# Kernel optimization log

Hardware: AMD Instinct MI355X
Metric: run time of the kernel (lower is better)

## Reference

```python
import jax, jax.numpy as jnp
import numpy as np

B, N, IN_DIM, OUT_DIM, H = 8, 1024, 256, 256, 4
HD = OUT_DIM // H  # head_dim = 64
NEG = -1e9
EPS = 1e-5


def setup_inputs() -> dict:
    key = jax.random.key(0)
    ks = jax.random.split(key, 9)
    h = jax.random.normal(ks[0], (B, N, IN_DIM), dtype=jnp.float32)
    adj = jax.random.randint(ks[1], (N, N), 0, 2, dtype=jnp.int32)
    adj = adj.at[jnp.arange(N), jnp.arange(N)].set(1)  # self loops so no empty rows
    s = 1.0 / np.sqrt(IN_DIM)
    W = jax.random.uniform(ks[2], (H, IN_DIM, HD), jnp.float32, -s, s)
    sa = 1.0 / np.sqrt(2 * HD)
    a1 = jax.random.uniform(ks[3], (H, HD), jnp.float32, -sa, sa)
    a2 = jax.random.uniform(ks[4], (H, HD), jnp.float32, -sa, sa)
    sp = 1.0 / np.sqrt(OUT_DIM)
    proj_w = jax.random.uniform(ks[5], (OUT_DIM, OUT_DIM), jnp.float32, -sp, sp)
    proj_b = jax.random.uniform(ks[6], (OUT_DIM,), jnp.float32, -sp, sp)
    gamma = jnp.ones((OUT_DIM,), jnp.float32)
    beta = jnp.zeros((OUT_DIM,), jnp.float32)
    return {"h": h, "adj": adj, "W": W, "a1": a1, "a2": a2,
            "proj_w": proj_w, "proj_b": proj_b, "gamma": gamma, "beta": beta}


def reference(h, adj, W, a1, a2, proj_w, proj_b, gamma, beta):
    # Wh: [B,H,N,HD]
    Wh = jnp.einsum('bni,hid->bhnd', h, W)
    # Decompose a([Wh_i || Wh_j]) = a1.Wh_i + a2.Wh_j (same math as concat+linear)
    si = jnp.einsum('bhnd,hd->bhn', Wh, a1)  # [B,H,N]
    sj = jnp.einsum('bhnd,hd->bhn', Wh, a2)
    e = jax.nn.leaky_relu(si[:, :, :, None] + sj[:, :, None, :], 0.2)  # [B,H,N,N]
    mask = (adj == 0)  # [N,N]
    e = jnp.where(mask[None, None], NEG, e)
    alpha = jax.nn.softmax(e, axis=-1)
    out = jnp.einsum('bhnm,bhmd->bhnd', alpha, Wh)  # [B,H,N,HD]
    h_multi = out.transpose(0, 2, 1, 3).reshape(B, N, OUT_DIM)  # concat heads
    h_out = jnp.einsum('bnd,od->bno', h_multi, proj_w) + proj_b
    h_out = h_out + h  # residual (in_dim == out_dim)
    mu = jnp.mean(h_out, axis=-1, keepdims=True)
    var = jnp.mean(jnp.square(h_out - mu), axis=-1, keepdims=True)
    return (h_out - mu) * jax.lax.rsqrt(var + EPS) * gamma + beta
```

## Files before the change

kernel.cpp:

```cpp
#include <hip/hip_runtime.h>
#include <hip/hip_bf16.h>

#define NN 1024
#define LOG2E 1.44269504088896f

typedef __attribute__((ext_vector_type(8))) short short8;
typedef __attribute__((ext_vector_type(4))) float floatx4;
typedef __attribute__((ext_vector_type(4))) int intx4;
typedef __attribute__((ext_vector_type(2))) int intx2;

#define WAIT_VM0()   asm volatile("s_waitcnt vmcnt(0)" ::: "memory")
#define WAIT_VM4()   asm volatile("s_waitcnt vmcnt(4)" ::: "memory")
#define WAIT_LGKM0() asm volatile("s_waitcnt lgkmcnt(0)" ::: "memory")
#define SCHED_FENCE() asm volatile("" ::: "memory")

static __device__ __forceinline__ unsigned pk2(float f0, float f1) {
    unsigned u0 = __float_as_uint(f0) + 0x8000u;
    unsigned u1 = __float_as_uint(f1) + 0x8000u;
    return __builtin_amdgcn_perm(u1, u0, 0x07060302u);
}
static __device__ __forceinline__ short8 pk8(floatx4 v0, floatx4 v1) {
    union { intx4 i; short8 s; } u;
    u.i[0] = (int)pk2(v0[0], v0[1]); u.i[1] = (int)pk2(v0[2], v0[3]);
    u.i[2] = (int)pk2(v1[0], v1[1]); u.i[3] = (int)pk2(v1[2], v1[3]);
    return u.s;
}
static __device__ __forceinline__ void load_lds16(const void* gsrc, void* lds) {
    __builtin_amdgcn_global_load_lds(
        (const __attribute__((address_space(1))) void*)gsrc,
        (__attribute__((address_space(3))) void*)lds, 16, 0, 0);
}

__global__ __launch_bounds__(256) void prep_kernel(
    const float* __restrict__ W, const float* __restrict__ proj_w,
    const int* __restrict__ adj,
    __hip_bfloat16* __restrict__ WTb,
    __hip_bfloat16* __restrict__ pwb,
    unsigned* __restrict__ adjm)
{
    int blk = blockIdx.x, t = threadIdx.x;
    if (blk < 16) {
        int o = blk * 16 + (t >> 4);
        int hh = o >> 6, d = o & 63;
        #pragma unroll
        for (int kk = 0; kk < 16; ++kk) {
            int k = (t & 15) + 16 * kk;
            WTb[(size_t)o * 256 + k] = __float2bfloat16(W[((size_t)hh * 256 + k) * 64 + d]);
        }
    } else if (blk < 32) {
        size_t base = (size_t)(blk - 16) * 4096 + (size_t)t * 16;
        #pragma unroll
        for (int k = 0; k < 16; k += 8) {
            floatx4 v0 = *(const floatx4*)(proj_w + base + k);
            floatx4 v1 = *(const floatx4*)(proj_w + base + k + 4);
            *(short8*)(pwb + base + k) = pk8(v0, v1);
        }
    } else {
        int n = (blk - 32) * 8 + (t >> 5);
        int wd = t & 31;
        const int* arow = adj + (size_t)n * NN + wd * 32;
        unsigned bits = 0;
        #pragma unroll
        for (int j4 = 0; j4 < 8; ++j4) {
            intx4 v = *(const intx4*)(arow + j4 * 4);
            #pragma unroll
            for (int j = 0; j < 4; ++j) if (v[j] != 0) bits |= (1u << (j4 * 4 + j));
        }
        adjm[(size_t)n * 32 + wd] = bits;
    }
}

__global__ __launch_bounds__(512) void wh_kernel(
    const float* __restrict__ h,
    const __hip_bfloat16* __restrict__ WTb,
    const float* __restrict__ a1, const float* __restrict__ a2,
    __hip_bfloat16* __restrict__ WhTt,
    float* __restrict__ si, float* __restrict__ sj)
{
    __shared__ __align__(16) __hip_bfloat16 WTbs[8][4096];
    __shared__ float redsi[2][4][4][16];
    __shared__ float redsj[2][4][4][16];

    int t = threadIdx.x;
    int w = t >> 6, l = t & 63;
    int rt = w >> 2, ds = w & 3;
    int rl = l & 15, q = l >> 4;
    int bx = blockIdx.x;
    int bb = bx >> 5, tb = bx & 31;

    short8 af[8];
    const float* Arow = h + ((size_t)bb * 1024 + tb * 32 + rt * 16 + rl) * 256 + q * 8;
    #pragma unroll
    for (int k0 = 0; k0 < 8; ++k0) {
        floatx4 v0 = *(const floatx4*)(Arow + k0 * 32);
        floatx4 v1 = *(const floatx4*)(Arow + k0 * 32 + 4);
        af[k0] = pk8(v0, v1);
    }

    int d = ds * 16 + rl;
    int s = rt * 16 + q * 4;
    size_t toff = (size_t)d * 32 + (((s >> 3) ^ (d & 3)) * 8) + (s & 7);
    int srow_ = l >> 5;

    #pragma unroll
    for (int ph = 0; ph < 2; ++ph) {
        if (ph) __syncthreads();
        #pragma unroll
        for (int k = 0; k < 8; ++k) {
            int row = k * 2 + srow_;
            int g = (l & 31) ^ (row & 7);
            load_lds16(WTb + (size_t)(ph * 128 + w * 16 + row) * 256 + g * 8, &WTbs[w][k * 512]);
        }
        __syncthreads();

        #pragma unroll
        for (int jj = 0; jj < 2; ++jj) {
            int head = ph * 2 + jj;
            int lt = ds + 4 * jj;
            floatx4 acc = {0.f, 0.f, 0.f, 0.f};
            #pragma unroll
            for (int k0 = 0; k0 < 8; ++k0) {
                int p = ((k0 << 2) + q) ^ (rl & 7);
                short8 bf = *(const short8*)(&WTbs[lt][rl * 256 + p * 8]);
                acc = __builtin_amdgcn_mfma_f32_16x16x32_bf16(af[k0], bf, acc, 0, 0, 0);
            }

            intx2 pr;
            pr[0] = (int)pk2(acc[0], acc[1]);
            pr[1] = (int)pk2(acc[2], acc[3]);
            *(intx2*)(WhTt + ((size_t)(bb * 4 + head) * 32 + tb) * 2048 + toff) = pr;

            float av1 = a1[head * 64 + d] * LOG2E;
            float av2 = a2[head * 64 + d] * LOG2E;
            #pragma unroll
            for (int i = 0; i < 4; ++i) {
                float p1 = acc[i] * av1, p2 = acc[i] * av2;
                #pragma unroll
                for (int off = 1; off < 16; off <<= 1) {
                    p1 += __shfl_xor(p1, off, 64);
                    p2 += __shfl_xor(p2, off, 64);
                }
                if (rl == 0) { redsi[rt][ds][head][q * 4 + i] = p1; redsj[rt][ds][head][q * 4 + i] = p2; }
            }
        }
    }
    __syncthreads();

    if (t < 128) {
        int head = t >> 5, u = t & 31, rt2 = u >> 4, row = u & 15;
        si[(size_t)(bb * 4 + head) * NN + tb * 32 + rt2 * 16 + row] =
            redsi[rt2][0][head][row] + redsi[rt2][1][head][row] +
            redsi[rt2][2][head][row] + redsi[rt2][3][head][row];
    } else if (t < 256) {
        int u2 = t - 128;
        int head = u2 >> 5, u = u2 & 31, rt2 = u >> 4, row = u & 15;
        sj[(size_t)(bb * 4 + head) * NN + tb * 32 + rt2 * 16 + row] =
            redsj[rt2][0][head][row] + redsj[rt2][1][head][row] +
            redsj[rt2][2][head][row] + redsj[rt2][3][head][row];
    }
}

__global__ __launch_bounds__(512, 4) void attn_proj_kernel(
    const unsigned* __restrict__ adjm,
    const __hip_bfloat16* __restrict__ WhTt,
    const float* __restrict__ si, const float* __restrict__ sj,
    const __hip_bfloat16* __restrict__ pwb,
    const float* __restrict__ h,
    const float* __restrict__ proj_b, const float* __restrict__ gamma,
    const float* __restrict__ beta,
    float* __restrict__ out)
{
    __shared__ __align__(16) char smem[76288];
    auto bst   = reinterpret_cast<__hip_bfloat16 (*)[2][2048]>(smem);
    auto pl    = reinterpret_cast<__hip_bfloat16 (*)[16][40]>(smem + 65536);
    auto hm    = reinterpret_cast<__hip_bfloat16 (*)[264]>(smem + 65536);
    auto red   = reinterpret_cast<float (*)[8][16]>(smem + 65536 + 8448);
    auto lsums = reinterpret_cast<float (*)[4][16]>(smem + 75776);
    float (*accx)[64][20] = reinterpret_cast<float (*)[64][20]>(smem);

    int bx = blockIdx.x, t = threadIdx.x;
    int w = t >> 6, l = t & 63;
    int hh = w & 3, e = w >> 2;
    int rl = l & 15, q = l >> 4;
    int b = bx >> 6, n0 = (bx & 63) * 16;
    int bh = b * 4 + hh;
    int r0 = bx * 16;

    int r = l >> 2, cg = l & 3;
    float sii = si[(size_t)bh * NN + n0 + r];
    const float* sjr = sj + (size_t)bh * NN;
    const unsigned* amrow = adjm + (size_t)(n0 + r) * 32;

    float lsum = 0.f;
    floatx4 acc[4] = { {0,0,0,0}, {0,0,0,0}, {0,0,0,0}, {0,0,0,0} };

    const __hip_bfloat16* Tbase = WhTt + ((size_t)bh * 32 + e) * 2048 + l * 8;

    #pragma unroll
    for (int k = 0; k < 4; ++k)
        load_lds16(Tbase + k * 512, &bst[w][0][k * 512]);

    #pragma unroll 2
    for (int it = 0; it < 16; ++it) {
        int buf = it & 1;
        int mw = it * 64 + e * 32;
        {
            unsigned bits = amrow[it * 2 + e] >> (cg * 8);
            int mb = mw + cg * 8;
            #pragma unroll
            for (int c4 = 0; c4 < 2; ++c4) {
                floatx4 s4 = *(const floatx4*)(sjr + mb + c4 * 4);
                float pv[4];
                #pragma unroll
                for (int k = 0; k < 4; ++k) {
                    float x = sii + s4[k];
                    x = fmaxf(x, 0.2f * x);
                    x = ((bits >> (c4 * 4 + k)) & 1u) ? x : -1e9f;
                    pv[k] = exp2f(x);
                    lsum += pv[k];
                }
                intx2 two;
                two[0] = (int)pk2(pv[0], pv[1]);
                two[1] = (int)pk2(pv[2], pv[3]);
                *(intx2*)(&pl[w][r][cg * 8 + c4 * 4]) = two;
            }
        }
        SCHED_FENCE();
        if (it < 15) {
            const __hip_bfloat16* Tn = Tbase + (size_t)(it + 1) * 2 * 2048;
            #pragma unroll
            for (int k = 0; k < 4; ++k)
                load_lds16(Tn + k * 512, &bst[w][buf ^ 1][k * 512]);
            WAIT_VM4();
        } else {
            WAIT_VM0();
        }
        short8 afr = *(const short8*)(&pl[w][rl][q * 8]);
        #pragma unroll
        for (int dt = 0; dt < 4; ++dt) {
            short8 bfr = *(const short8*)(&bst[w][buf][(dt * 16 + rl) * 32 + (q ^ (rl & 3)) * 8]);
            acc[dt] = __builtin_amdgcn_mfma_f32_16x16x32_bf16(afr, bfr, acc[dt], 0, 0, 0);
        }
    }

    lsum += __shfl_xor(lsum, 1, 64);
    lsum += __shfl_xor(lsum, 2, 64);
    if (cg == 0) lsums[e][hh][r] = lsum;

    __syncthreads();

    if (e == 1) {
        #pragma unroll
        for (int dt = 0; dt < 4; ++dt) {
            #pragma unroll
            for (int i = 0; i < 4; ++i)
                accx[hh][l][dt * 4 + i] = acc[dt][i];
        }
    }
    __syncthreads();

    if (e == 0) {
        float riv[4];
        #pragma unroll
        for (int i = 0; i < 4; ++i)
            riv[i] = 1.f / (lsums[0][hh][q * 4 + i] + lsums[1][hh][q * 4 + i]);
        #pragma unroll
        for (int dt = 0; dt < 4; ++dt) {
            #pragma unroll
            for (int i = 0; i < 4; ++i) {
                float v = acc[dt][i] + accx[hh][l][dt * 4 + i];
                unsigned uv = (__float_as_uint(v * riv[i]) + 0x8000u) >> 16;
                hm[q * 4 + i][hh * 64 + dt * 16 + rl] = __ushort_as_bfloat16((unsigned short)uv);
            }
        }
    }
    __syncthreads();

    short8 paf[8];
    #pragma unroll
    for (int k0 = 0; k0 < 8; ++k0) paf[k0] = *(const short8*)(&hm[rl][q * 8 + k0 * 32]);

    floatx4 pacc[2];
    #pragma unroll
    for (int j = 0; j < 2; ++j) {
        int ct = w + 8 * j;
        const __hip_bfloat16* Bp = pwb + (size_t)(ct * 16 + rl) * 256 + q * 8;
        floatx4 a = {0.f, 0.f, 0.f, 0.f};
        #pragma unroll
        for (int k0 = 0; k0 < 8; ++k0) {
            short8 bfp = *(const short8*)(Bp + k0 * 32);
            a = __builtin_amdgcn_mfma_f32_16x16x32_bf16(paf[k0], bfp, a, 0, 0, 0);
        }
        pacc[j] = a;
    }

    float ps[4] = {0.f, 0.f, 0.f, 0.f};
    #pragma unroll
    for (int j = 0; j < 2; ++j) {
        int col = (w + 8 * j) * 16 + rl;
        float pb = proj_b[col];
        #pragma unroll
        for (int i = 0; i < 4; ++i) {
            float v = pacc[j][i] + pb + h[(size_t)(r0 + q * 4 + i) * 256 + col];
            pacc[j][i] = v;
            ps[i] += v;
        }
    }
    #pragma unroll
    for (int i = 0; i < 4; ++i) {
        float s = ps[i];
        #pragma unroll
        for (int off = 1; off < 16; off <<= 1) s += __shfl_xor(s, off, 64);
        ps[i] = s;
    }
    if (rl == 0) {
        for (int i = 0; i < 4; ++i) red[0][w][q * 4 + i] = ps[i];
    }
    __syncthreads();
    float mu[4];
    #pragma unroll
    for (int i = 0; i < 4; ++i) {
        int row = q * 4 + i;
        float s = 0.f;
        #pragma unroll
        for (int ww = 0; ww < 8; ++ww) s += red[0][ww][row];
        mu[i] = s * (1.f / 256.f);
    }
    float vs[4] = {0.f, 0.f, 0.f, 0.f};
    #pragma unroll
    for (int j = 0; j < 2; ++j) {
        #pragma unroll
        for (int i = 0; i < 4; ++i) { float cv = pacc[j][i] - mu[i]; vs[i] += cv * cv; }
    }
    #pragma unroll
    for (int i = 0; i < 4; ++i) {
        float s = vs[i];
        #pragma unroll
        for (int off = 1; off < 16; off <<= 1) s += __shfl_xor(s, off, 64);
        vs[i] = s;
    }
    if (rl == 0) {
        for (int i = 0; i < 4; ++i) red[1][w][q * 4 + i] = vs[i];
    }
    __syncthreads();
    float rs[4];
    #pragma unroll
    for (int i = 0; i < 4; ++i) {
        int row = q * 4 + i;
        float s = 0.f;
        #pragma unroll
        for (int ww = 0; ww < 8; ++ww) s += red[1][ww][row];
        rs[i] = rsqrtf(s * (1.f / 256.f) + 1e-5f);
    }
    #pragma unroll
    for (int j = 0; j < 2; ++j) {
        int col = (w + 8 * j) * 16 + rl;
        float g = gamma[col], be = beta[col];
        #pragma unroll
        for (int i = 0; i < 4; ++i)
            out[(size_t)(r0 + q * 4 + i) * 256 + col] = (pacc[j][i] - mu[i]) * rs[i] * g + be;
    }
}

extern "C" void kernel_launch(void* const* d_in, const int* in_sizes, int n_in,
                              void* d_out, int out_size, void* d_ws, size_t ws_size,
                              hipStream_t stream) {
    const float* h      = (const float*)d_in[0];
    const int*   adj    = (const int*)d_in[1];
    const float* W      = (const float*)d_in[2];
    const float* a1     = (const float*)d_in[3];
    const float* a2     = (const float*)d_in[4];
    const float* proj_w = (const float*)d_in[5];
    const float* proj_b = (const float*)d_in[6];
    const float* gamma  = (const float*)d_in[7];
    const float* beta   = (const float*)d_in[8];
    float* out = (float*)d_out;

    char* ws = (char*)d_ws;
    __hip_bfloat16* WhTt = (__hip_bfloat16*)ws;  ws += (size_t)32 * 32 * 2048 * 2;
    __hip_bfloat16* WTb = (__hip_bfloat16*)ws;   ws += 256 * 256 * 2;
    __hip_bfloat16* pwb = (__hip_bfloat16*)ws;   ws += 256 * 256 * 2;
    float* si = (float*)ws;                      ws += (size_t)32 * NN * 4;
    float* sj = (float*)ws;                      ws += (size_t)32 * NN * 4;
    unsigned* adjm = (unsigned*)ws;              ws += (size_t)NN * 32 * 4;

    prep_kernel<<<160, 256, 0, stream>>>(W, proj_w, adj, WTb, pwb, adjm);
    wh_kernel<<<256, 512, 0, stream>>>(h, WTb, a1, a2, WhTt, si, sj);
    attn_proj_kernel<<<512, 512, 0, stream>>>(adjm, WhTt, si, sj, pwb, h, proj_b, gamma, beta, out);
}
```

Before: 120.5 us.

## Split fused attention+projection into per-head attention and separate projection kernels

The fused attention/projection kernel becomes two kernels. The new attention kernel runs one block per (batch, head, 16-row tile), giving 2048 blocks of 256 threads; each wave covers a quarter of the key range, and the partial accumulators are reduced through LDS. B fragments now load straight from global into registers, replacing the asynchronous LDS double-buffering, and the adjacency bitmask is stored transposed so the per-row word loads coalesce. Normalized bf16 head outputs go to a global buffer that a separate projection+LayerNorm kernel reads. This adds parallelism but costs an extra launch, a global round trip for the intermediate, and the loss of explicit load/compute overlap.

Measured after the change: 125.4 us. 4.1% more time.

```diff
diff --git a/kernel.cpp b/kernel.cpp
--- a/kernel.cpp
+++ b/kernel.cpp
@@ -8,11 +8,6 @@
 typedef __attribute__((ext_vector_type(4))) float floatx4;
 typedef __attribute__((ext_vector_type(4))) int intx4;
 typedef __attribute__((ext_vector_type(2))) int intx2;
-
-#define WAIT_VM0()   asm volatile("s_waitcnt vmcnt(0)" ::: "memory")
-#define WAIT_VM4()   asm volatile("s_waitcnt vmcnt(4)" ::: "memory")
-#define WAIT_LGKM0() asm volatile("s_waitcnt lgkmcnt(0)" ::: "memory")
-#define SCHED_FENCE() asm volatile("" ::: "memory")
 
 static __device__ __forceinline__ unsigned pk2(float f0, float f1) {
     unsigned u0 = __float_as_uint(f0) + 0x8000u;
@@ -36,7 +31,7 @@
     const int* __restrict__ adj,
     __hip_bfloat16* __restrict__ WTb,
     __hip_bfloat16* __restrict__ pwb,
-    unsigned* __restrict__ adjm)
+    unsigned* __restrict__ adjT)
 {
     int blk = blockIdx.x, t = threadIdx.x;
     if (blk < 16) {
@@ -66,7 +61,7 @@
             #pragma unroll
             for (int j = 0; j < 4; ++j) if (v[j] != 0) bits |= (1u << (j4 * 4 + j));
         }
-        adjm[(size_t)n * 32 + wd] = bits;
+        adjT[(size_t)wd * NN + n] = bits;
     }
 }
 
@@ -160,130 +155,121 @@
     }
 }
 
-__global__ __launch_bounds__(512, 4) void attn_proj_kernel(
-    const unsigned* __restrict__ adjm,
+__global__ __launch_bounds__(256, 4) void attn_kernel(
+    const unsigned* __restrict__ adjT,
     const __hip_bfloat16* __restrict__ WhTt,
     const float* __restrict__ si, const float* __restrict__ sj,
+    __hip_bfloat16* __restrict__ hmg)
+{
+    __shared__ __align__(16) __hip_bfloat16 pl[4][16][72];
+    __shared__ float accs[4][64][17];
+    __shared__ float lsums[4][16];
+
+    int bx = blockIdx.x, t = threadIdx.x;
+    int w = t >> 6, l = t & 63;
+    int rl = l & 15, q = l >> 4;
+    int head = bx & 3, tile = (bx >> 2) & 63, b = bx >> 8;
+    int n0 = tile * 16;
+    int bh = b * 4 + head;
+    int r = l >> 2, cg = l & 3;
+    int nr = n0 + r;
+
+    float sii = si[(size_t)bh * NN + nr];
+    const float* sjr = sj + (size_t)bh * NN;
+    const __hip_bfloat16* Tbh = WhTt + (size_t)bh * 32 * 2048;
+
+    float lsum = 0.f;
+    floatx4 acc[4] = { {0,0,0,0}, {0,0,0,0}, {0,0,0,0}, {0,0,0,0} };
+
+    #pragma unroll 2
+    for (int it = 0; it < 4; ++it) {
+        int mabs = w * 256 + it * 64;
+        int t0 = mabs >> 5;
+        short8 bf[8];
+        #pragma unroll
+        for (int ks = 0; ks < 2; ++ks) {
+            #pragma unroll
+            for (int dt = 0; dt < 4; ++dt)
+                bf[ks * 4 + dt] = *(const short8*)(Tbh + (size_t)(t0 + ks) * 2048
+                                    + (dt * 16 + rl) * 32 + ((q ^ (rl & 3)) * 8));
+        }
+        unsigned wA = adjT[(size_t)t0 * NN + nr];
+        unsigned wB = adjT[(size_t)(t0 + 1) * NN + nr];
+        unsigned half = (cg < 2 ? wA : wB) >> ((cg & 1) * 16);
+        int mb = mabs + cg * 16;
+        #pragma unroll
+        for (int c4 = 0; c4 < 4; ++c4) {
+            floatx4 s4 = *(const floatx4*)(sjr + mb + c4 * 4);
+            float pv[4];
+            #pragma unroll
+            for (int k = 0; k < 4; ++k) {
+                float x = sii + s4[k];
+                x = fmaxf(x, 0.2f * x);
+                x = ((half >> (c4 * 4 + k)) & 1u) ? x : -1e9f;
+                pv[k] = exp2f(x);
+                lsum += pv[k];
+            }
+            intx2 two;
+            two[0] = (int)pk2(pv[0], pv[1]);
+            two[1] = (int)pk2(pv[2], pv[3]);
+            *(intx2*)(&pl[w][r][cg * 16 + c4 * 4]) = two;
+        }
+        #pragma unroll
+        for (int ks = 0; ks < 2; ++ks) {
+            short8 afr = *(const short8*)(&pl[w][rl][ks * 32 + q * 8]);
+            #pragma unroll
+            for (int dt = 0; dt < 4; ++dt)
+                acc[dt] = __builtin_amdgcn_mfma_f32_16x16x32_bf16(afr, bf[ks * 4 + dt], acc[dt], 0, 0, 0);
+        }
+    }
+
+    lsum += __shfl_xor(lsum, 1, 64);
+    lsum += __shfl_xor(lsum, 2, 64);
+    if (cg == 0) lsums[w][r] = lsum;
+    #pragma unroll
+    for (int dt = 0; dt < 4; ++dt) {
+        #pragma unroll
+        for (int i = 0; i < 4; ++i)
+            accs[w][l][dt * 4 + i] = acc[dt][i];
+    }
+    __syncthreads();
+
+    #pragma unroll
+    for (int i = 0; i < 4; ++i) {
+        int row = q * 4 + i;
+        float riv = 1.f / (lsums[0][row] + lsums[1][row] + lsums[2][row] + lsums[3][row]);
+        float cc = accs[0][l][w * 4 + i] + accs[1][l][w * 4 + i]
+                 + accs[2][l][w * 4 + i] + accs[3][l][w * 4 + i];
+        unsigned uv = (__float_as_uint(cc * riv) + 0x8000u) >> 16;
+        hmg[(size_t)(b * 1024 + n0 + row) * 256 + head * 64 + w * 16 + rl]
+            = __ushort_as_bfloat16((unsigned short)uv);
+    }
+}
+
+__global__ __launch_bounds__(256) void proj_kernel(
+    const __hip_bfloat16* __restrict__ hmg,
     const __hip_bfloat16* __restrict__ pwb,
     const float* __restrict__ h,
     const float* __restrict__ proj_b, const float* __restrict__ gamma,
     const float* __restrict__ beta,
     float* __restrict__ out)
 {
-    __shared__ __align__(16) char smem[76288];
-    auto bst   = reinterpret_cast<__hip_bfloat16 (*)[2][2048]>(smem);
-    auto pl    = reinterpret_cast<__hip_bfloat16 (*)[16][40]>(smem + 65536);
-    auto hm    = reinterpret_cast<__hip_bfloat16 (*)[264]>(smem + 65536);
-    auto red   = reinterpret_cast<float (*)[8][16]>(smem + 65536 + 8448);
-    auto lsums = reinterpret_cast<float (*)[4][16]>(smem + 75776);
-    float (*accx)[64][20] = reinterpret_cast<float (*)[64][20]>(smem);
+    __shared__ float red[2][4][16];
 
     int bx = blockIdx.x, t = threadIdx.x;
     int w = t >> 6, l = t & 63;
-    int hh = w & 3, e = w >> 2;
     int rl = l & 15, q = l >> 4;
-    int b = bx >> 6, n0 = (bx & 63) * 16;
-    int bh = b * 4 + hh;
     int r0 = bx * 16;
 
-    int r = l >> 2, cg = l & 3;
-    float sii = si[(size_t)bh * NN + n0 + r];
-    const float* sjr = sj + (size_t)bh * NN;
-    const unsigned* amrow = adjm + (size_t)(n0 + r) * 32;
-
-    float lsum = 0.f;
-    floatx4 acc[4] = { {0,0,0,0}, {0,0,0,0}, {0,0,0,0}, {0,0,0,0} };
-
-    const __hip_bfloat16* Tbase = WhTt + ((size_t)bh * 32 + e) * 2048 + l * 8;
-
-    #pragma unroll
-    for (int k = 0; k < 4; ++k)
-        load_lds16(Tbase + k * 512, &bst[w][0][k * 512]);
-
-    #pragma unroll 2
-    for (int it = 0; it < 16; ++it) {
-        int buf = it & 1;
-        int mw = it * 64 + e * 32;
-        {
-            unsigned bits = amrow[it * 2 + e] >> (cg * 8);
-            int mb = mw + cg * 8;
-            #pragma unroll
-            for (int c4 = 0; c4 < 2; ++c4) {
-                floatx4 s4 = *(const floatx4*)(sjr + mb + c4 * 4);
-                float pv[4];
-                #pragma unroll
-                for (int k = 0; k < 4; ++k) {
-                    float x = sii + s4[k];
-                    x = fmaxf(x, 0.2f * x);
-                    x = ((bits >> (c4 * 4 + k)) & 1u) ? x : -1e9f;
-                    pv[k] = exp2f(x);
-                    lsum += pv[k];
-                }
-                intx2 two;
-                two[0] = (int)pk2(pv[0], pv[1]);
-                two[1] = (int)pk2(pv[2], pv[3]);
-                *(intx2*)(&pl[w][r][cg * 8 + c4 * 4]) = two;
-            }
-        }
-        SCHED_FENCE();
-        if (it < 15) {
-            const __hip_bfloat16* Tn = Tbase + (size_t)(it + 1) * 2 * 2048;
-            #pragma unroll
-            for (int k = 0; k < 4; ++k)
-                load_lds16(Tn + k * 512, &bst[w][buf ^ 1][k * 512]);
-            WAIT_VM4();
-        } else {
-            WAIT_VM0();
-        }
-        short8 afr = *(const short8*)(&pl[w][rl][q * 8]);
-        #pragma unroll
-        for (int dt = 0; dt < 4; ++dt) {
-            short8 bfr = *(const short8*)(&bst[w][buf][(dt * 16 + rl) * 32 + (q ^ (rl & 3)) * 8]);
-            acc[dt] = __builtin_amdgcn_mfma_f32_16x16x32_bf16(afr, bfr, acc[dt], 0, 0, 0);
-        }
-    }
-
-    lsum += __shfl_xor(lsum, 1, 64);
-    lsum += __shfl_xor(lsum, 2, 64);
-    if (cg == 0) lsums[e][hh][r] = lsum;
-
-    __syncthreads();
-
-    if (e == 1) {
-        #pragma unroll
-        for (int dt = 0; dt < 4; ++dt) {
-            #pragma unroll
-            for (int i = 0; i < 4; ++i)
-                accx[hh][l][dt * 4 + i] = acc[dt][i];
-        }
-    }
-    __syncthreads();
-
-    if (e == 0) {
-        float riv[4];
-        #pragma unroll
-        for (int i = 0; i < 4; ++i)
-            riv[i] = 1.f / (lsums[0][hh][q * 4 + i] + lsums[1][hh][q * 4 + i]);
-        #pragma unroll
-        for (int dt = 0; dt < 4; ++dt) {
-            #pragma unroll
-            for (int i = 0; i < 4; ++i) {
-                float v = acc[dt][i] + accx[hh][l][dt * 4 + i];
-                unsigned uv = (__float_as_uint(v * riv[i]) + 0x8000u) >> 16;
-                hm[q * 4 + i][hh * 64 + dt * 16 + rl] = __ushort_as_bfloat16((unsigned short)uv);
-            }
-        }
-    }
-    __syncthreads();
-
     short8 paf[8];
     #pragma unroll
-    for (int k0 = 0; k0 < 8; ++k0) paf[k0] = *(const short8*)(&hm[rl][q * 8 + k0 * 32]);
-
-    floatx4 pacc[2];
-    #pragma unroll
-    for (int j = 0; j < 2; ++j) {
-        int ct = w + 8 * j;
+    for (int k0 = 0; k0 < 8; ++k0)
+        paf[k0] = *(const short8*)(hmg + (size_t)(r0 + rl) * 256 + q * 8 + k0 * 32);
+
+    floatx4 pacc[4];
+    #pragma unroll
+    for (int j = 0; j < 4; ++j) {
+        int ct = w + 4 * j;
         const __hip_bfloat16* Bp = pwb + (size_t)(ct * 16 + rl) * 256 + q * 8;
         floatx4 a = {0.f, 0.f, 0.f, 0.f};
         #pragma unroll
@@ -296,8 +282,8 @@
 
     float ps[4] = {0.f, 0.f, 0.f, 0.f};
     #pragma unroll
-    for (int j = 0; j < 2; ++j) {
-        int col = (w + 8 * j) * 16 + rl;
+    for (int j = 0; j < 4; ++j) {
+        int col = (w + j * 4) * 16 + rl;
         float pb = proj_b[col];
         #pragma unroll
         for (int i = 0; i < 4; ++i) {
@@ -321,14 +307,11 @@
     #pragma unroll
     for (int i = 0; i < 4; ++i) {
         int row = q * 4 + i;
-        float s = 0.f;
-        #pragma unroll
-        for (int ww = 0; ww < 8; ++ww) s += red[0][ww][row];
-        mu[i] = s * (1.f / 256.f);
+        mu[i] = (red[0][0][row] + red[0][1][row] + red[0][2][row] + red[0][3][row]) * (1.f / 256.f);
     }
     float vs[4] = {0.f, 0.f, 0.f, 0.f};
     #pragma unroll
-    for (int j = 0; j < 2; ++j) {
+    for (int j = 0; j < 4; ++j) {
         #pragma unroll
         for (int i = 0; i < 4; ++i) { float cv = pacc[j][i] - mu[i]; vs[i] += cv * cv; }
     }
@@ -347,14 +330,12 @@
     #pragma unroll
     for (int i = 0; i < 4; ++i) {
         int row = q * 4 + i;
-        float s = 0.f;
-        #pragma unroll
-        for (int ww = 0; ww < 8; ++ww) s += red[1][ww][row];
-        rs[i] = rsqrtf(s * (1.f / 256.f) + 1e-5f);
-    }
-    #pragma unroll
-    for (int j = 0; j < 2; ++j) {
-        int col = (w + 8 * j) * 16 + rl;
+        float var = (red[1][0][row] + red[1][1][row] + red[1][2][row] + red[1][3][row]) * (1.f / 256.f);
+        rs[i] = rsqrtf(var + 1e-5f);
+    }
+    #pragma unroll
+    for (int j = 0; j < 4; ++j) {
+        int col = (w + j * 4) * 16 + rl;
         float g = gamma[col], be = beta[col];
         #pragma unroll
         for (int i = 0; i < 4; ++i)
@@ -382,9 +363,11 @@
     __hip_bfloat16* pwb = (__hip_bfloat16*)ws;   ws += 256 * 256 * 2;
     float* si = (float*)ws;                      ws += (size_t)32 * NN * 4;
     float* sj = (float*)ws;                      ws += (size_t)32 * NN * 4;
-    unsigned* adjm = (unsigned*)ws;              ws += (size_t)NN * 32 * 4;
-
-    prep_kernel<<<160, 256, 0, stream>>>(W, proj_w, adj, WTb, pwb, adjm);
+    unsigned* adjT = (unsigned*)ws;              ws += (size_t)NN * 32 * 4;
+    __hip_bfloat16* hmg = (__hip_bfloat16*)ws;   ws += (size_t)8 * NN * 256 * 2;
+
+    prep_kernel<<<160, 256, 0, stream>>>(W, proj_w, adj, WTb, pwb, adjT);
     wh_kernel<<<256, 512, 0, stream>>>(h, WTb, a1, a2, WhTt, si, sj);
-    attn_proj_kernel<<<512, 512, 0, stream>>>(adjm, WhTt, si, sj, pwb, h, proj_b, gamma, beta, out);
-}
+    attn_kernel<<<2048, 256, 0, stream>>>(adjT, WhTt, si, sj, hmg);
+    proj_kernel<<<512, 256, 0, stream>>>(hmg, pwb, h, proj_b, gamma, beta, out);
+}
```
